# Kernel tuning notes

Hardware: AMD Instinct MI355X
Metric: run time of the kernel (lower is better)

## Reference

```python
import jax, jax.numpy as jnp
import numpy as np

NODE_DIM = 128
HIDDEN = 64
N_NODES = 100000
N_REL = 50
N_EDGES = 1000000
TEMPERATURE = 0.5
BIAS = 1e-4


def _xavier(key, shape):
    fan_in, fan_out = shape[0], shape[1]
    lim = jnp.sqrt(6.0 / (fan_in + fan_out))
    return jax.random.uniform(key, shape, jnp.float32, -lim, lim)


def setup_inputs() -> dict:
    key = jax.random.key(0)
    ks = jax.random.split(key, 16)
    inp = {
        "edge_index": jax.random.randint(ks[0], (2, N_EDGES), 0, N_NODES),
        "edge_type": jax.random.randint(ks[1], (N_EDGES,), 0, N_REL),
        "all_embed": jax.random.normal(ks[2], (N_NODES, NODE_DIM), jnp.float32),
        "relation_emb": jax.random.normal(ks[3], (N_REL, NODE_DIM), jnp.float32),
        "u": jax.random.uniform(ks[4], (N_EDGES,), jnp.float32),
    }
    # four 2-layer MLPs: Linear(node_dim, hidden) -> ReLU -> Linear(hidden, 1)
    names = ["src", "dst", "edge", "con"]
    for i, nm in enumerate(names):
        k1, k2 = jax.random.split(ks[5 + i])
        inp[f"W1_{nm}"] = _xavier(k1, (NODE_DIM, HIDDEN))
        inp[f"b1_{nm}"] = jnp.zeros((HIDDEN,), jnp.float32)
        inp[f"W2_{nm}"] = _xavier(k2, (HIDDEN, 1))
        inp[f"b2_{nm}"] = jnp.zeros((1,), jnp.float32)
    return inp


def _mlp(x, W1, b1, W2, b2):
    # x: [E, node_dim] -> [E, 1]
    h = jnp.maximum(x @ W1 + b1, 0.0)
    return h @ W2 + b2


def reference(edge_index, edge_type, all_embed, relation_emb, u,
              W1_src, b1_src, W2_src, b2_src,
              W1_dst, b1_dst, W2_dst, b2_dst,
              W1_edge, b1_edge, W2_edge, b2_edge,
              W1_con, b1_con, W2_con, b2_con):
    head = all_embed[edge_index[0]]          # [E, D] gather
    tail = all_embed[edge_index[1]]          # [E, D] gather
    latent = relation_emb[edge_type]         # [E, D] gather

    weight = _mlp(head + tail + latent, W1_con, b1_con, W2_con, b2_con)
    weight = weight + _mlp(head, W1_src, b1_src, W2_src, b2_src)
    weight = weight + _mlp(tail, W1_dst, b1_dst, W2_dst, b2_dst)
    weight = weight + _mlp(latent, W1_edge, b1_edge, W2_edge, b2_edge)
    weight = weight[:, 0]                    # squeeze -> [E]

    # eps = (bias - (1-bias)) * u + (1-bias), bias = 1e-4
    eps = (2.0 * BIAS - 1.0) * u + (1.0 - BIAS)
    gate_inputs = jnp.log(eps) - jnp.log1p(-eps)
    gate_inputs = (gate_inputs + weight) / TEMPERATURE
    return jax.nn.sigmoid(gate_inputs)       # [E]
```

## Files before the change

kernel.cpp:

```cpp
#include <hip/hip_runtime.h>
#include <hip/hip_bf16.h>
#include <hip/hip_fp16.h>
#include <math.h>

#define NODE_DIM 128
#define HIDDEN   64
#define N_NODES  100000
#define N_RELS   50
#define N_EDGESC 1000000
#define TEMPERATURE 0.5f
#define BIASF 0.0001f

typedef __attribute__((ext_vector_type(8))) _Float16 f16x8;
typedef __attribute__((ext_vector_type(4))) float    f32x4;

__global__ __launch_bounds__(256) void prep_small(
    const float* __restrict__ W1c, const float* __restrict__ W1s,
    const float* __restrict__ W1d,
    const float* __restrict__ rel_emb,
    const float* __restrict__ b1c,
    const float* __restrict__ W1e, const float* __restrict__ b1e,
    const float* __restrict__ W2e, const float* __restrict__ b2e,
    const float* __restrict__ b2c,
    _Float16* __restrict__ wt,
    float* __restrict__ qcon, float* __restrict__ srel) {
  const int bid = blockIdx.x;
  if (bid < 96) {
    const int tid = bid * 256 + threadIdx.x;
    const int k = tid / 192;
    const int n = tid % 192;
    const float* W = (n < 64) ? W1c : (n < 128) ? W1s : W1d;
    const float v = W[k * HIDDEN + (n & 63)];
    const int ks = k ^ ((n & 7) << 3);
    wt[n * NODE_DIM + ks] = (_Float16)v;
  } else {
    const int r = (bid - 96) * 4 + (threadIdx.x >> 6);
    const int l = threadIdx.x & 63;
    if (r >= N_RELS) return;
    const float* x = rel_emb + (size_t)r * NODE_DIM;
    float ac = 0.f, ae = 0.f;
    #pragma unroll 8
    for (int k = 0; k < NODE_DIM; ++k) {
      float xk = x[k];
      ac = fmaf(xk, W1c[k * HIDDEN + l], ac);
      ae = fmaf(xk, W1e[k * HIDDEN + l], ae);
    }
    qcon[r * HIDDEN + l] = ac + b1c[l];
    float he = fmaxf(ae + b1e[l], 0.f) * W2e[l];
    #pragma unroll
    for (int off = 32; off > 0; off >>= 1) he += __shfl_xor(he, off);
    if (l == 0) srel[r] = he + b2e[0] + b2c[0];
  }
}

__global__ __launch_bounds__(512) void prep_gemm(
    const float* __restrict__ x,
    const _Float16* __restrict__ wt,
    const float* __restrict__ b1s, const float* __restrict__ W2s,
    const float* __restrict__ b2s,
    const float* __restrict__ b1d, const float* __restrict__ W2d,
    const float* __restrict__ b2d,
    __half* __restrict__ pcon,
    float* __restrict__ ssrc, float* __restrict__ sdst) {
  __shared__ _Float16 bl[192 * NODE_DIM];
  const int wv = threadIdx.x >> 6;
  const int l  = threadIdx.x & 63;
  const int hi = l >> 4;
  const int c  = l & 15;

  {
    const char* g = (const char*)wt;
    #pragma unroll
    for (int i = 0; i < 6; ++i) {
      const int chunk = (i * 8 + wv) << 10;
      __builtin_amdgcn_global_load_lds(
          (const __attribute__((address_space(1))) void*)(g + chunk + l * 16),
          (__attribute__((address_space(3))) void*)((char*)bl + chunk),
          16, 0, 0);
    }
  }

  const int m0   = blockIdx.x * 128 + wv * 16;
  const int arow = m0 + c;
  const int rowc = arow < N_NODES ? arow : N_NODES - 1;
  const float* xr = x + (size_t)rowc * NODE_DIM + hi * 8;
  f16x8 a[4];
  #pragma unroll
  for (int s = 0; s < 4; ++s) {
    float4 u0 = *(const float4*)(xr + s * 32);
    float4 u1 = *(const float4*)(xr + s * 32 + 4);
    f16x8 av;
    av[0] = (_Float16)u0.x; av[1] = (_Float16)u0.y;
    av[2] = (_Float16)u0.z; av[3] = (_Float16)u0.w;
    av[4] = (_Float16)u1.x; av[5] = (_Float16)u1.y;
    av[6] = (_Float16)u1.z; av[7] = (_Float16)u1.w;
    a[s] = av;
  }

  __syncthreads();

  f32x4 acc[12];
  #pragma unroll
  for (int i = 0; i < 12; ++i) acc[i] = (f32x4){0.f, 0.f, 0.f, 0.f};

  #pragma unroll
  for (int tt = 0; tt < 12; ++tt) {
    const int n = tt * 16 + c;
    const int nbase = n * NODE_DIM;
    #pragma unroll
    for (int s = 0; s < 4; ++s) {
      const int ks = (s * 32 + hi * 8) ^ ((n & 7) << 3);
      f16x8 b = *(const f16x8*)(&bl[nbase + ks]);
      acc[tt] = __builtin_amdgcn_mfma_f32_16x16x32_f16(a[s], b, acc[tt], 0, 0, 0);
    }
  }

  #pragma unroll
  for (int tt = 0; tt < 4; ++tt) {
    #pragma unroll
    for (int g = 0; g < 4; ++g) {
      const int row = m0 + hi * 4 + g;
      if (row < N_NODES)
        pcon[(size_t)row * HIDDEN + tt * 16 + c] = __float2half(acc[tt][g]);
    }
  }
  float ps[4] = {0.f, 0.f, 0.f, 0.f};
  float pd[4] = {0.f, 0.f, 0.f, 0.f};
  #pragma unroll
  for (int tt = 0; tt < 4; ++tt) {
    const int h = tt * 16 + c;
    const float b1sv = b1s[h], w2sv = W2s[h];
    const float b1dv = b1d[h], w2dv = W2d[h];
    #pragma unroll
    for (int g = 0; g < 4; ++g) {
      ps[g] += fmaxf(acc[4 + tt][g] + b1sv, 0.f) * w2sv;
      pd[g] += fmaxf(acc[8 + tt][g] + b1dv, 0.f) * w2dv;
    }
  }
  #pragma unroll
  for (int off = 1; off < 16; off <<= 1) {
    #pragma unroll
    for (int g = 0; g < 4; ++g) {
      ps[g] += __shfl_xor(ps[g], off);
      pd[g] += __shfl_xor(pd[g], off);
    }
  }
  if (c == 0) {
    const float bs = b2s[0], bd = b2d[0];
    #pragma unroll
    for (int g = 0; g < 4; ++g) {
      const int row = m0 + hi * 4 + g;
      if (row < N_NODES) { ssrc[row] = ps[g] + bs; sdst[row] = pd[g] + bd; }
    }
  }
}

__global__ __launch_bounds__(256) void edge_kernel(
    const int*   __restrict__ edge_index,
    const int*   __restrict__ edge_type,
    const float* __restrict__ u,
    const __half* __restrict__ pcon,
    const float* __restrict__ ssrc,
    const float* __restrict__ sdst,
    const float* __restrict__ qcon,
    const float* __restrict__ srel,
    const float* __restrict__ W2c,
    float* __restrict__ out) {
  const int tid = blockIdx.x * 256 + threadIdx.x;
  const int e   = tid >> 3;
  const int sub = tid & 7;

  const int src = edge_index[e];
  const int dst = edge_index[N_EDGESC + e];
  const int r   = edge_type[e];

  const int soff = src * HIDDEN + sub * 8;
  const int doff = dst * HIDDEN + sub * 8;

  uint4 us = *(const uint4*)(pcon + soff);
  uint4 ut = *(const uint4*)(pcon + doff);
  const float4 q0 = *(const float4*)(qcon + r * HIDDEN + sub * 8);
  const float4 q1 = *(const float4*)(qcon + r * HIDDEN + sub * 8 + 4);
  const float4 w0 = *(const float4*)(W2c + sub * 8);
  const float4 w1 = *(const float4*)(W2c + sub * 8 + 4);

  const __half2* hs = (const __half2*)&us;
  const __half2* ht = (const __half2*)&ut;
  const float qv[8] = {q0.x, q0.y, q0.z, q0.w, q1.x, q1.y, q1.z, q1.w};
  const float wv[8] = {w0.x, w0.y, w0.z, w0.w, w1.x, w1.y, w1.z, w1.w};

  float s = 0.f;
  #pragma unroll
  for (int j = 0; j < 4; ++j) {
    float2 fs = __half22float2(hs[j]);
    float2 ft = __half22float2(ht[j]);
    s += fmaxf(fs.x + ft.x + qv[2 * j],     0.f) * wv[2 * j];
    s += fmaxf(fs.y + ft.y + qv[2 * j + 1], 0.f) * wv[2 * j + 1];
  }
  s += __shfl_xor(s, 1);
  s += __shfl_xor(s, 2);
  s += __shfl_xor(s, 4);

  if (sub == 0) {
    float wsum = s + ssrc[src] + sdst[dst] + srel[r];
    float uu   = u[e];
    float eps  = fmaf(2.f * BIASF - 1.f, uu, 1.f - BIASF);
    float ome  = fmaf(1.f - 2.f * BIASF, uu, BIASF);
    float g    = __logf(eps) - __logf(ome);
    float z    = (g + wsum) * (1.f / TEMPERATURE);
    out[e] = __builtin_amdgcn_rcpf(1.f + __expf(-z));
  }
}

extern "C" void kernel_launch(void* const* d_in, const int* in_sizes, int n_in,
                              void* d_out, int out_size, void* d_ws, size_t ws_size,
                              hipStream_t stream) {
  const int*   edge_index = (const int*)d_in[0];
  const int*   edge_type  = (const int*)d_in[1];
  const float* all_embed  = (const float*)d_in[2];
  const float* rel_emb    = (const float*)d_in[3];
  const float* u          = (const float*)d_in[4];
  const float* W1_src = (const float*)d_in[5];
  const float* b1_src = (const float*)d_in[6];
  const float* W2_src = (const float*)d_in[7];
  const float* b2_src = (const float*)d_in[8];
  const float* W1_dst = (const float*)d_in[9];
  const float* b1_dst = (const float*)d_in[10];
  const float* W2_dst = (const float*)d_in[11];
  const float* b2_dst = (const float*)d_in[12];
  const float* W1_edge = (const float*)d_in[13];
  const float* b1_edge = (const float*)d_in[14];
  const float* W2_edge = (const float*)d_in[15];
  const float* b2_edge = (const float*)d_in[16];
  const float* W1_con = (const float*)d_in[17];
  const float* b1_con = (const float*)d_in[18];
  const float* W2_con = (const float*)d_in[19];
  const float* b2_con = (const float*)d_in[20];

  char* ws = (char*)d_ws;
  __half*   pcon = (__half*)ws;
  float*    ssrc = (float*)(ws + (size_t)N_NODES * HIDDEN * 2);
  float*    sdst = ssrc + N_NODES;
  float*    qcon = sdst + N_NODES;
  float*    srel = qcon + N_RELS * HIDDEN;
  _Float16* wt   = (_Float16*)(srel + N_RELS);

  prep_small<<<96 + (N_RELS + 3) / 4, 256, 0, stream>>>(
      W1_con, W1_src, W1_dst, rel_emb, b1_con,
      W1_edge, b1_edge, W2_edge, b2_edge, b2_con,
      wt, qcon, srel);

  prep_gemm<<<(N_NODES + 127) / 128, 512, 0, stream>>>(
      all_embed, wt,
      b1_src, W2_src, b2_src, b1_dst, W2_dst, b2_dst,
      pcon, ssrc, sdst);

  edge_kernel<<<(N_EDGESC * 8) / 256, 256, 0, stream>>>(
      edge_index, edge_type, u, pcon, ssrc, sdst, qcon, srel, W2_con,
      (float*)d_out);
}
```

Before: 71.14 us.

## Process one edge per thread with packed fp16 math and fdot2 reduction

```diff
diff --git a/kernel.cpp b/kernel.cpp
--- a/kernel.cpp
+++ b/kernel.cpp
@@ -12,7 +12,10 @@
 #define BIASF 0.0001f
 
 typedef __attribute__((ext_vector_type(8))) _Float16 f16x8;
+typedef __attribute__((ext_vector_type(2))) _Float16 hv2;
 typedef __attribute__((ext_vector_type(4))) float    f32x4;
+
+union U4 { uint4 u; hv2 h[4]; };
 
 __global__ __launch_bounds__(256) void prep_small(
     const float* __restrict__ W1c, const float* __restrict__ W1s,
@@ -21,9 +24,10 @@
     const float* __restrict__ b1c,
     const float* __restrict__ W1e, const float* __restrict__ b1e,
     const float* __restrict__ W2e, const float* __restrict__ b2e,
-    const float* __restrict__ b2c,
+    const float* __restrict__ b2c, const float* __restrict__ W2c,
     _Float16* __restrict__ wt,
-    float* __restrict__ qcon, float* __restrict__ srel) {
+    _Float16* __restrict__ qh, float* __restrict__ srel,
+    _Float16* __restrict__ w2h) {
   const int bid = blockIdx.x;
   if (bid < 96) {
     const int tid = bid * 256 + threadIdx.x;
@@ -34,6 +38,8 @@
     const int ks = k ^ ((n & 7) << 3);
     wt[n * NODE_DIM + ks] = (_Float16)v;
   } else {
+    if (bid == 96 && threadIdx.x < HIDDEN)
+      w2h[threadIdx.x] = (_Float16)W2c[threadIdx.x];
     const int r = (bid - 96) * 4 + (threadIdx.x >> 6);
     const int l = threadIdx.x & 63;
     if (r >= N_RELS) return;
@@ -45,7 +51,7 @@
       ac = fmaf(xk, W1c[k * HIDDEN + l], ac);
       ae = fmaf(xk, W1e[k * HIDDEN + l], ae);
     }
-    qcon[r * HIDDEN + l] = ac + b1c[l];
+    qh[r * HIDDEN + l] = (_Float16)(ac + b1c[l]);
     float he = fmaxf(ae + b1e[l], 0.f) * W2e[l];
     #pragma unroll
     for (int off = 32; off > 0; off >>= 1) he += __shfl_xor(he, off);
@@ -159,57 +165,50 @@
     const int*   __restrict__ edge_index,
     const int*   __restrict__ edge_type,
     const float* __restrict__ u,
-    const __half* __restrict__ pcon,
+    const _Float16* __restrict__ pcon,
     const float* __restrict__ ssrc,
     const float* __restrict__ sdst,
-    const float* __restrict__ qcon,
+    const _Float16* __restrict__ qh,
     const float* __restrict__ srel,
-    const float* __restrict__ W2c,
+    const _Float16* __restrict__ w2h,
     float* __restrict__ out) {
-  const int tid = blockIdx.x * 256 + threadIdx.x;
-  const int e   = tid >> 3;
-  const int sub = tid & 7;
+  const int e = blockIdx.x * 256 + threadIdx.x;
+  if (e >= N_EDGESC) return;
 
   const int src = edge_index[e];
   const int dst = edge_index[N_EDGESC + e];
   const int r   = edge_type[e];
-
-  const int soff = src * HIDDEN + sub * 8;
-  const int doff = dst * HIDDEN + sub * 8;
-
-  uint4 us = *(const uint4*)(pcon + soff);
-  uint4 ut = *(const uint4*)(pcon + doff);
-  const float4 q0 = *(const float4*)(qcon + r * HIDDEN + sub * 8);
-  const float4 q1 = *(const float4*)(qcon + r * HIDDEN + sub * 8 + 4);
-  const float4 w0 = *(const float4*)(W2c + sub * 8);
-  const float4 w1 = *(const float4*)(W2c + sub * 8 + 4);
-
-  const __half2* hs = (const __half2*)&us;
-  const __half2* ht = (const __half2*)&ut;
-  const float qv[8] = {q0.x, q0.y, q0.z, q0.w, q1.x, q1.y, q1.z, q1.w};
-  const float wv[8] = {w0.x, w0.y, w0.z, w0.w, w1.x, w1.y, w1.z, w1.w};
-
-  float s = 0.f;
-  #pragma unroll
-  for (int j = 0; j < 4; ++j) {
-    float2 fs = __half22float2(hs[j]);
-    float2 ft = __half22float2(ht[j]);
-    s += fmaxf(fs.x + ft.x + qv[2 * j],     0.f) * wv[2 * j];
-    s += fmaxf(fs.y + ft.y + qv[2 * j + 1], 0.f) * wv[2 * j + 1];
-  }
-  s += __shfl_xor(s, 1);
-  s += __shfl_xor(s, 2);
-  s += __shfl_xor(s, 4);
-
-  if (sub == 0) {
-    float wsum = s + ssrc[src] + sdst[dst] + srel[r];
-    float uu   = u[e];
-    float eps  = fmaf(2.f * BIASF - 1.f, uu, 1.f - BIASF);
-    float ome  = fmaf(1.f - 2.f * BIASF, uu, BIASF);
-    float g    = __logf(eps) - __logf(ome);
-    float z    = (g + wsum) * (1.f / TEMPERATURE);
-    out[e] = __builtin_amdgcn_rcpf(1.f + __expf(-z));
-  }
+  const float uu = u[e];
+
+  const uint4* Sp = (const uint4*)(pcon + src * HIDDEN);
+  const uint4* Dp = (const uint4*)(pcon + dst * HIDDEN);
+  const uint4* Qp = (const uint4*)(qh + r * HIDDEN);
+  const uint4* Wp = (const uint4*)w2h;
+
+  U4 S[8], D[8], Q[8], W[8];
+  #pragma unroll
+  for (int k = 0; k < 8; ++k) { S[k].u = Sp[k]; D[k].u = Dp[k]; }
+  #pragma unroll
+  for (int k = 0; k < 8; ++k) { Q[k].u = Qp[k]; W[k].u = Wp[k]; }
+  const float sadd = ssrc[src] + sdst[dst] + srel[r];
+
+  float acc = 0.f;
+  #pragma unroll
+  for (int k = 0; k < 8; ++k) {
+    #pragma unroll
+    for (int j = 0; j < 4; ++j) {
+      hv2 h = S[k].h[j] + D[k].h[j] + Q[k].h[j];
+      h = __builtin_elementwise_max(h, (hv2)(_Float16)0.f);
+      acc = __builtin_amdgcn_fdot2(h, W[k].h[j], acc, false);
+    }
+  }
+
+  const float wsum = acc + sadd;
+  const float eps  = fmaf(2.f * BIASF - 1.f, uu, 1.f - BIASF);
+  const float ome  = fmaf(1.f - 2.f * BIASF, uu, BIASF);
+  const float g    = __logf(eps) - __logf(ome);
+  const float z    = (g + wsum) * (1.f / TEMPERATURE);
+  out[e] = __builtin_amdgcn_rcpf(1.f + __expf(-z));
 }
 
 extern "C" void kernel_launch(void* const* d_in, const int* in_sizes, int n_in,
@@ -238,24 +237,25 @@
   const float* b2_con = (const float*)d_in[20];
 
   char* ws = (char*)d_ws;
-  __half*   pcon = (__half*)ws;
+  _Float16* pcon = (_Float16*)ws;
   float*    ssrc = (float*)(ws + (size_t)N_NODES * HIDDEN * 2);
   float*    sdst = ssrc + N_NODES;
-  float*    qcon = sdst + N_NODES;
-  float*    srel = qcon + N_RELS * HIDDEN;
-  _Float16* wt   = (_Float16*)(srel + N_RELS);
+  _Float16* wt   = (_Float16*)(sdst + N_NODES);
+  _Float16* qh   = wt + 192 * NODE_DIM;
+  _Float16* w2h  = qh + N_RELS * HIDDEN;
+  float*    srel = (float*)(w2h + HIDDEN);
 
   prep_small<<<96 + (N_RELS + 3) / 4, 256, 0, stream>>>(
       W1_con, W1_src, W1_dst, rel_emb, b1_con,
-      W1_edge, b1_edge, W2_edge, b2_edge, b2_con,
-      wt, qcon, srel);
+      W1_edge, b1_edge, W2_edge, b2_edge, b2_con, W2_con,
+      wt, qh, srel, w2h);
 
   prep_gemm<<<(N_NODES + 127) / 128, 512, 0, stream>>>(
       all_embed, wt,
       b1_src, W2_src, b2_src, b1_dst, W2_dst, b2_dst,
-      pcon, ssrc, sdst);
-
-  edge_kernel<<<(N_EDGESC * 8) / 256, 256, 0, stream>>>(
-      edge_index, edge_type, u, pcon, ssrc, sdst, qcon, srel, W2_con,
+      (__half*)pcon, ssrc, sdst);
+
+  edge_kernel<<<(N_EDGESC + 255) / 256, 256, 0, stream>>>(
+      edge_index, edge_type, u, pcon, ssrc, sdst, qh, srel, w2h,
       (float*)d_out);
 }
```

Measured after the change: 102.8 us. 1.44x slower.
